# Kernel tuning notes

Hardware: AMD Instinct MI355X
Metric: run time of the kernel (lower is better)

## Reference

```python
import jax, jax.numpy as jnp
import numpy as np

N_NODES = 100000
N_EDGES = 1000000
NUM_FEATURES = 64
HIDDEN = 64
NUM_GRAPHS = 128


def setup_inputs() -> dict:
    key = jax.random.key(0)
    ks = jax.random.split(key, 12)
    x = jax.random.normal(ks[0], (N_NODES, NUM_FEATURES), dtype=jnp.float32)
    edge_index = jax.random.randint(ks[1], (2, N_EDGES), 0, N_NODES, dtype=jnp.int64)
    edge_weight = jax.random.uniform(ks[2], (N_EDGES,), dtype=jnp.float32)
    batch = jnp.sort(jax.random.randint(ks[3], (N_NODES,), 0, NUM_GRAPHS, dtype=jnp.int64))
    s1 = 1.0 / np.sqrt(NUM_FEATURES)
    s2 = 1.0 / np.sqrt(HIDDEN)
    # GraphConv layer 1: lin_rel (with bias) applied to aggregated msgs, lin_root (no bias)
    w1_rel = jax.random.uniform(ks[4], (HIDDEN, NUM_FEATURES), jnp.float32, -s1, s1)
    b1_rel = jax.random.uniform(ks[5], (HIDDEN,), jnp.float32, -s1, s1)
    w1_root = jax.random.uniform(ks[6], (HIDDEN, NUM_FEATURES), jnp.float32, -s1, s1)
    # GraphConv layer 2
    w2_rel = jax.random.uniform(ks[7], (HIDDEN, HIDDEN), jnp.float32, -s2, s2)
    b2_rel = jax.random.uniform(ks[8], (HIDDEN,), jnp.float32, -s2, s2)
    w2_root = jax.random.uniform(ks[9], (HIDDEN, HIDDEN), jnp.float32, -s2, s2)
    # final Linear(hidden, 1)
    w_lin = jax.random.uniform(ks[10], (1, HIDDEN), jnp.float32, -s2, s2)
    b_lin = jax.random.uniform(ks[11], (1,), jnp.float32, -s2, s2)
    return {
        "x": x, "edge_index": edge_index, "edge_weight": edge_weight, "batch": batch,
        "w1_rel": w1_rel, "b1_rel": b1_rel, "w1_root": w1_root,
        "w2_rel": w2_rel, "b2_rel": b2_rel, "w2_root": w2_root,
        "w_lin": w_lin, "b_lin": b_lin,
    }


def graph_conv(x, edge_index, edge_weight, w_rel, b_rel, w_root):
    # messages: x[src] * e, scatter-add into dst  (gather-scale-scatter)
    src, dst = edge_index[0], edge_index[1]
    msgs = x[src] * edge_weight[:, None]                      # [E, F]
    aggr = jax.ops.segment_sum(msgs, dst, num_segments=x.shape[0])  # [N, F]
    return aggr @ w_rel.T + b_rel + x @ w_root.T


def reference(x, edge_index, edge_weight, batch,
              w1_rel, b1_rel, w1_root, w2_rel, b2_rel, w2_root, w_lin, b_lin):
    h = graph_conv(x, edge_index, edge_weight, w1_rel, b1_rel, w1_root)
    h = jax.nn.relu(h)
    h = graph_conv(h, edge_index, edge_weight, w2_rel, b2_rel, w2_root)
    # global_mean_pool over graph ids
    sums = jax.ops.segment_sum(h, batch, num_segments=NUM_GRAPHS)          # [G, H]
    counts = jax.ops.segment_sum(jnp.ones((h.shape[0],), h.dtype), batch,
                                 num_segments=NUM_GRAPHS)                  # [G]
    pooled = sums / jnp.maximum(counts, 1.0)[:, None]
    # dropout(p=0.5) in eval mode is identity
    return pooled @ w_lin.T + b_lin                                        # [G, 1]
```

## Files before the change

### kernel.cpp

```cpp
#include <hip/hip_runtime.h>
#include <hip/hip_bf16.h>


#define N_NODES 100000
#define N_EDGES 1000000
#define NGRAPHS 128
#define BN 512
#define NBUCK ((N_NODES + BN - 1) / BN)
#define FILL_T 16
#define FILL_TILE (256 * FILL_T)
#define FILL_NB ((N_EDGES + FILL_TILE - 1) / FILL_TILE)
#define NTILES (N_NODES / 16)
#define AST 72
#define CVT_NB 3126
#define HIST_NB 256

typedef __attribute__((ext_vector_type(8))) short bf16x8;
typedef __attribute__((ext_vector_type(8))) unsigned short u16x8;
typedef __attribute__((ext_vector_type(4))) float f32x4;

__device__ __forceinline__ unsigned short f2bf(float f) {
    unsigned u = __float_as_uint(f);
    unsigned r = (u + 0x7FFFu + ((u >> 16) & 1u)) >> 16;
    return (unsigned short)r;
}
__device__ __forceinline__ float bf2f(unsigned short h) {
    return __uint_as_float(((unsigned)h) << 16);
}

__global__ __launch_bounds__(256) void prep_cvt_hist_kernel(
    const float* __restrict__ x, unsigned short* __restrict__ xh, int n8,
    const float* __restrict__ w1rel, const float* __restrict__ w1root,
    const float* __restrict__ w2rel, const float* __restrict__ w2root,
    const float* __restrict__ wlin, const float* __restrict__ b2rel,
    const float* __restrict__ blin, unsigned short* __restrict__ whirel,
    unsigned short* __restrict__ wlorel, unsigned short* __restrict__ whiroot,
    unsigned short* __restrict__ wloroot, float* __restrict__ u,
    float* __restrict__ v, float* __restrict__ C,
    const int* __restrict__ ei, int* __restrict__ bcount, int E) {
    int tid = threadIdx.x;
    if (blockIdx.x >= CVT_NB) {
        __shared__ int lh[NBUCK];
        for (int i = tid; i < NBUCK; i += 256) lh[i] = 0;
        __syncthreads();
        int bid2 = blockIdx.x - CVT_NB;
        for (int e = bid2 * 256 + tid; e < E; e += HIST_NB * 256)
            atomicAdd(&lh[ei[E + e] >> 9], 1);
        __syncthreads();
        for (int i = tid; i < NBUCK; i += 256) {
            int c = lh[i];
            if (c) atomicAdd(&bcount[i], c);
        }
        return;
    }
    int i = blockIdx.x * 256 + tid;
    if (i < n8) {
        const float4* xp = (const float4*)x + (size_t)i * 2;
        float4 a = xp[0], b = xp[1];
        u16x8 o;
        o[0] = f2bf(a.x); o[1] = f2bf(a.y); o[2] = f2bf(a.z); o[3] = f2bf(a.w);
        o[4] = f2bf(b.x); o[5] = f2bf(b.y); o[6] = f2bf(b.z); o[7] = f2bf(b.w);
        *((u16x8*)xh + i) = o;
        return;
    }
    for (int k = tid; k < 4096; k += 256) {
        float a = w1rel[k];
        unsigned short hi = f2bf(a);
        whirel[k] = hi;
        wlorel[k] = f2bf(a - bf2f(hi));
        float b = w1root[k];
        unsigned short hb = f2bf(b);
        whiroot[k] = hb;
        wloroot[k] = f2bf(b - bf2f(hb));
    }
    if (tid < 64) {
        float uu = 0.f, vv = 0.f;
        for (int h = 0; h < 64; ++h) {
            float wl = wlin[h];
            uu += wl * w2rel[h * 64 + tid];
            vv += wl * w2root[h * 64 + tid];
        }
        u[tid] = uu;
        v[tid] = vv;
    }
    if (tid == 0) {
        float c = blin[0];
        for (int h = 0; h < 64; ++h) c += wlin[h] * b2rel[h];
        *C = c;
    }
}

__global__ void bucket_scan(const int* __restrict__ bcount,
                            int* __restrict__ boff, int* __restrict__ cursor) {
    __shared__ int s[256];
    int t = threadIdx.x;
    int v = (t < NBUCK) ? bcount[t] : 0;
    s[t] = v;
    __syncthreads();
    for (int off = 1; off < 256; off <<= 1) {
        int x = (t >= off) ? s[t - off] : 0;
        __syncthreads();
        s[t] += x;
        __syncthreads();
    }
    if (t < NBUCK) {
        boff[t] = s[t] - v;
        cursor[t] = s[t] - v;
    }
    if (t == 255) boff[NBUCK] = s[255];
}

__global__ __launch_bounds__(256) void bucket_fill(
    const int* __restrict__ ei, const float* __restrict__ ew,
    int* __restrict__ cursor, int2* __restrict__ ebuf, int E) {
    __shared__ int lh[NBUCK];
    __shared__ int gbase[NBUCK];
    int tid = threadIdx.x;
    for (int i = tid; i < NBUCK; i += 256) lh[i] = 0;
    __syncthreads();
    int base = blockIdx.x * FILL_TILE;
    int2 rec[FILL_T];
    int meta[FILL_T];
#pragma unroll
    for (int i = 0; i < FILL_T; ++i) {
        int e = base + i * 256 + tid;
        meta[i] = -1;
        if (e < E) {
            int src = ei[e];
            int dst = ei[E + e];
            int b = dst >> 9;
            int r = atomicAdd(&lh[b], 1);
            rec[i].x = src | ((dst & (BN - 1)) << 17);
            rec[i].y = __float_as_int(ew[e]);
            meta[i] = (b << 13) | r;
        }
    }
    __syncthreads();
    for (int i = tid; i < NBUCK; i += 256) {
        int c = lh[i];
        gbase[i] = c ? atomicAdd(&cursor[i], c) : 0;
    }
    __syncthreads();
#pragma unroll
    for (int i = 0; i < FILL_T; ++i) {
        if (meta[i] >= 0) {
            int b = meta[i] >> 13;
            int r = meta[i] & 8191;
            ebuf[gbase[b] + r] = rec[i];
        }
    }
}

__global__ __launch_bounds__(512) void csr_build(
    const int* __restrict__ boff, const int2* __restrict__ ebuf,
    const int* __restrict__ batch, int* __restrict__ row_ptr,
    int2* __restrict__ csr, int N) {
    __shared__ int s[BN];
    int b = blockIdx.x;
    int t = threadIdx.x;
    int beg = boff[b], end = boff[b + 1];
    s[t] = 0;
    __syncthreads();
    for (int j = beg + t; j < end; j += 512)
        atomicAdd(&s[(ebuf[j].x >> 17) & (BN - 1)], 1);
    __syncthreads();
    int v = s[t];
    for (int off = 1; off < BN; off <<= 1) {
        int x = (t >= off) ? s[t - off] : 0;
        __syncthreads();
        s[t] += x;
        __syncthreads();
    }
    int excl = s[t] - v;
    int gidx = b * BN + t;
    if (gidx <= N) row_ptr[gidx] = beg + excl;
    __syncthreads();
    s[t] = excl;
    __syncthreads();
    for (int j = beg + t; j < end; j += 512) {
        int2 rec = ebuf[j];
        int dlo = (rec.x >> 17) & (BN - 1);
        int g = batch[b * BN + dlo];
        int r = atomicAdd(&s[dlo], 1);
        int2 o;
        o.x = (rec.x & 0x1FFFF) | (g << 17);
        o.y = rec.y;
        csr[beg + r] = o;
    }
}

__global__ __launch_bounds__(256) void gather_dense_kernel(
    const unsigned short* __restrict__ xh, const int* __restrict__ row_ptr,
    const int2* __restrict__ csr, const unsigned short* __restrict__ whirel,
    const unsigned short* __restrict__ wlorel,
    const unsigned short* __restrict__ whiroot,
    const unsigned short* __restrict__ wloroot,
    const float* __restrict__ b1rel, const float* __restrict__ u,
    const float* __restrict__ v, float* __restrict__ p, float* __restrict__ q,
    int ntiles) {
    __shared__ unsigned short arow[4][16 * AST];
    int lane = threadIdx.x & 63;
    int wv = threadIdx.x >> 6;
    int wave = (blockIdx.x << 2) + wv;
    if (wave >= ntiles) return;
    unsigned short* my = &arow[wv][0];
    int nb = wave * 16;
    int g = lane >> 3;
    int c = lane & 7;

#pragma unroll
    for (int r = 0; r < 2; ++r) {
        int node = nb + r * 8 + g;
        int beg = row_ptr[node], end = row_ptr[node + 1];
        float a0[8], a1[8];
#pragma unroll
        for (int t = 0; t < 8; ++t) { a0[t] = 0.f; a1[t] = 0.f; }
        int j = beg;
        for (; j + 2 <= end; j += 2) {
            int2 e0 = csr[j];
            int2 e1 = csr[j + 1];
            u16x8 x0 = *(const u16x8*)(xh + (size_t)(e0.x & 0x1FFFF) * 64 +
                                       c * 8);
            u16x8 x1 = *(const u16x8*)(xh + (size_t)(e1.x & 0x1FFFF) * 64 +
                                       c * 8);
            float w0 = __int_as_float(e0.y);
            float w1 = __int_as_float(e1.y);
#pragma unroll
            for (int t = 0; t < 8; ++t) {
                a0[t] += w0 * bf2f(x0[t]);
                a1[t] += w1 * bf2f(x1[t]);
            }
        }
        if (j < end) {
            int2 e0 = csr[j];
            u16x8 x0 = *(const u16x8*)(xh + (size_t)(e0.x & 0x1FFFF) * 64 +
                                       c * 8);
            float w0 = __int_as_float(e0.y);
#pragma unroll
            for (int t = 0; t < 8; ++t) a0[t] += w0 * bf2f(x0[t]);
        }
        u16x8 o;
#pragma unroll
        for (int t = 0; t < 8; ++t) o[t] = f2bf(a0[t] + a1[t]);
        *(u16x8*)(my + (r * 8 + g) * AST + c * 8) = o;
    }

    int lo4 = lane & 15;
    int quad = lane >> 4;
    f32x4 acc4[4];
#pragma unroll
    for (int t = 0; t < 4; ++t) acc4[t] = (f32x4){0.f, 0.f, 0.f, 0.f};
#pragma unroll
    for (int s = 0; s < 2; ++s) {
        bf16x8 Aa = *(const bf16x8*)(my + lo4 * AST + s * 32 + quad * 8);
        bf16x8 Ax = *(const bf16x8*)(xh + (size_t)(nb + lo4) * 64 + s * 32 +
                                     quad * 8);
#pragma unroll
        for (int t = 0; t < 4; ++t) {
            int off = (t * 16 + lo4) * 64 + s * 32 + quad * 8;
            bf16x8 bhr = *(const bf16x8*)(whirel + off);
            bf16x8 blr = *(const bf16x8*)(wlorel + off);
            bf16x8 bhx = *(const bf16x8*)(whiroot + off);
            bf16x8 blx = *(const bf16x8*)(wloroot + off);
            acc4[t] = __builtin_amdgcn_mfma_f32_16x16x32_bf16(Aa, bhr, acc4[t],
                                                              0, 0, 0);
            acc4[t] = __builtin_amdgcn_mfma_f32_16x16x32_bf16(Aa, blr, acc4[t],
                                                              0, 0, 0);
            acc4[t] = __builtin_amdgcn_mfma_f32_16x16x32_bf16(Ax, bhx, acc4[t],
                                                              0, 0, 0);
            acc4[t] = __builtin_amdgcn_mfma_f32_16x16x32_bf16(Ax, blx, acc4[t],
                                                              0, 0, 0);
        }
    }

    float pc[4] = {0.f, 0.f, 0.f, 0.f};
    float qc[4] = {0.f, 0.f, 0.f, 0.f};
#pragma unroll
    for (int t = 0; t < 4; ++t) {
        float bb = b1rel[t * 16 + lo4];
        float uu = u[t * 16 + lo4];
        float vv = v[t * 16 + lo4];
#pragma unroll
        for (int r = 0; r < 4; ++r) {
            float h1 = fmaxf(acc4[t][r] + bb, 0.f);
            pc[r] += uu * h1;
            qc[r] += vv * h1;
        }
    }
#pragma unroll
    for (int off = 1; off < 16; off <<= 1) {
#pragma unroll
        for (int r = 0; r < 4; ++r) {
            pc[r] += __shfl_xor(pc[r], off);
            qc[r] += __shfl_xor(qc[r], off);
        }
    }
    if (lo4 == 0) {
        f32x4 po = {pc[0], pc[1], pc[2], pc[3]};
        f32x4 qo = {qc[0], qc[1], qc[2], qc[3]};
        *(f32x4*)(p + nb + quad * 4) = po;
        *(f32x4*)(q + nb + quad * 4) = qo;
    }
}

#define PT_EPT 4
#define PT_EPW (64 * PT_EPT)
#define PT_NB ((N_EDGES + 4 * PT_EPW - 1) / (4 * PT_EPW))
#define PS_NB 98
__global__ __launch_bounds__(256) void pool_both(
    const int2* __restrict__ csr, const float* __restrict__ p,
    const float* __restrict__ q, const int* __restrict__ batch,
    float* __restrict__ gp, float* __restrict__ gq, float* __restrict__ gc,
    int* __restrict__ done, const float* __restrict__ C,
    float* __restrict__ out, int E, int N) {
    __shared__ float lbuf[2 * NGRAPHS];
    __shared__ int amLast;
    int tid = threadIdx.x;
    lbuf[tid] = 0.f;
    __syncthreads();
    if (blockIdx.x < PT_NB) {
        int lane = tid & 63;
        int wid = (blockIdx.x * 256 + tid) >> 6;
        int base = wid * PT_EPW;
        float acc = 0.f;
        int curg = -1;
#pragma unroll
        for (int i = 0; i < PT_EPT; ++i) {
            int j = base + i * 64 + lane;
            if (j < E) {
                int2 e = csr[j];
                int g = ((unsigned)e.x) >> 17;
                float val = __int_as_float(e.y) * p[e.x & 0x1FFFF];
                if (g != curg) {
                    if (curg >= 0) atomicAdd(&lbuf[curg], acc);
                    curg = g;
                    acc = 0.f;
                }
                acc += val;
            }
        }
        if (curg >= 0) atomicAdd(&lbuf[curg], acc);
        __syncthreads();
        if (tid < NGRAPHS) {
            float t = lbuf[tid];
            if (t != 0.f) atomicAdd(&gp[tid], t);
        }
    } else {
        int bid = blockIdx.x - PT_NB;
        for (int i = bid * 256 + tid; i < N; i += PS_NB * 256) {
            int g = batch[i];
            atomicAdd(&lbuf[g], q[i]);
            atomicAdd(&lbuf[NGRAPHS + g], 1.f);
        }
        __syncthreads();
        if (tid < NGRAPHS) {
            if (lbuf[NGRAPHS + tid] != 0.f) {
                atomicAdd(&gq[tid], lbuf[tid]);
                atomicAdd(&gc[tid], lbuf[NGRAPHS + tid]);
            }
        }
    }
    __syncthreads();
    if (tid == 0) {
        __threadfence();
        amLast = (atomicAdd(done, 1) == PT_NB + PS_NB - 1);
    }
    __syncthreads();
    if (amLast) {
        __threadfence();
        if (tid < NGRAPHS) {
            float pv = atomicAdd(&gp[tid], 0.f);
            float qv = atomicAdd(&gq[tid], 0.f);
            float cv = atomicAdd(&gc[tid], 0.f);
            out[tid] = (pv + qv) / fmaxf(cv, 1.f) + C[0];
        }
    }
}

extern "C" void kernel_launch(void* const* d_in, const int* in_sizes, int n_in,
                              void* d_out, int out_size, void* d_ws,
                              size_t ws_size, hipStream_t stream) {
    const float* x      = (const float*)d_in[0];
    const int*   ei     = (const int*)d_in[1];
    const float* ew     = (const float*)d_in[2];
    const int*   batch  = (const int*)d_in[3];
    const float* w1rel  = (const float*)d_in[4];
    const float* b1rel  = (const float*)d_in[5];
    const float* w1root = (const float*)d_in[6];
    const float* w2rel  = (const float*)d_in[7];
    const float* b2rel  = (const float*)d_in[8];
    const float* w2root = (const float*)d_in[9];
    const float* wlin   = (const float*)d_in[10];
    const float* blin   = (const float*)d_in[11];
    float* out = (float*)d_out;

    char* wsb = (char*)d_ws;
    int2* csr  = (int2*)wsb;
    int2* ebuf = (int2*)(wsb + (size_t)N_EDGES * 8);
    char* tail = wsb + (size_t)N_EDGES * 16;
    unsigned short* whirel  = (unsigned short*)tail;
    unsigned short* wlorel  = whirel + 4096;
    unsigned short* whiroot = wlorel + 4096;
    unsigned short* wloroot = whiroot + 4096;
    float* p  = (float*)(wloroot + 4096);
    float* q  = p + N_NODES;
    float* u  = q + N_NODES;
    float* v  = u + 64;
    float* C  = v + 64;
    int*   bcount = (int*)(C + 1);
    float* gp = (float*)(bcount + NBUCK);
    float* gq = gp + NGRAPHS;
    float* gc = gq + NGRAPHS;
    int*   done   = (int*)(gc + NGRAPHS);
    int*   boff   = done + 1;
    int*   cursor = boff + (NBUCK + 1);
    int*   row_ptr = cursor + NBUCK;
    unsigned short* xh = (unsigned short*)(row_ptr + N_NODES + 2);

    hipMemsetAsync(bcount, 0, (NBUCK + 3 * NGRAPHS + 1) * sizeof(int), stream);

    int n8 = N_NODES * 64 / 8;
    prep_cvt_hist_kernel<<<CVT_NB + HIST_NB, 256, 0, stream>>>(
        x, xh, n8, w1rel, w1root, w2rel, w2root, wlin, b2rel, blin, whirel,
        wlorel, whiroot, wloroot, u, v, C, ei, bcount, N_EDGES);

    bucket_scan<<<1, 256, 0, stream>>>(bcount, boff, cursor);
    bucket_fill<<<FILL_NB, 256, 0, stream>>>(ei, ew, cursor, ebuf, N_EDGES);
    csr_build<<<NBUCK, 512, 0, stream>>>(boff, ebuf, batch, row_ptr, csr,
                                         N_NODES);

    gather_dense_kernel<<<(NTILES + 3) / 4, 256, 0, stream>>>(
        xh, row_ptr, csr, whirel, wlorel, whiroot, wloroot, b1rel, u, v, p, q,
        NTILES);

    pool_both<<<PT_NB + PS_NB, 256, 0, stream>>>(csr, p, q, batch, gp, gq, gc,
                                                 done, C, out, N_EDGES,
                                                 N_NODES);
}
```

Measured before the change: 230.5 us.

## Gather neighbor features from an FP8 copy of x to halve gather bytes

Adds a kernel that converts the bf16 node features to FP8 (e4m3), written into the now-free edge staging buffer. The gather loop then reads 16 bytes of FP8 per lane with 4 lanes per node, instead of bf16 with 8 lanes per node, and unpacks with the hardware cvt_pk builtins. The aim is to cut random-gather memory traffic in the main aggregation. The cost is an extra kernel launch plus a conversion pass, and a large loss of precision in the aggregated features that may break the accuracy tolerance.

```diff
diff --git a/kernel.cpp b/kernel.cpp
--- a/kernel.cpp
+++ b/kernel.cpp
@@ -14,10 +14,12 @@
 #define AST 72
 #define CVT_NB 3126
 #define HIST_NB 256
+#define N16 (N_NODES * 64 / 16)
 
 typedef __attribute__((ext_vector_type(8))) short bf16x8;
 typedef __attribute__((ext_vector_type(8))) unsigned short u16x8;
 typedef __attribute__((ext_vector_type(4))) float f32x4;
+typedef __attribute__((ext_vector_type(2))) float f32x2;
 
 __device__ __forceinline__ unsigned short f2bf(float f) {
     unsigned u = __float_as_uint(f);
@@ -26,6 +28,19 @@
 }
 __device__ __forceinline__ float bf2f(unsigned short h) {
     return __uint_as_float(((unsigned)h) << 16);
+}
+__device__ __forceinline__ void fma4(int w, float wt, float* a) {
+    f32x2 lo = __builtin_amdgcn_cvt_pk_f32_fp8(w, false);
+    f32x2 hi = __builtin_amdgcn_cvt_pk_f32_fp8(w, true);
+    a[0] += wt * lo[0];
+    a[1] += wt * lo[1];
+    a[2] += wt * hi[0];
+    a[3] += wt * hi[1];
+}
+__device__ __forceinline__ int pack4(float f0, float f1, float f2, float f3) {
+    int w = __builtin_amdgcn_cvt_pk_fp8_f32(f0, f1, 0, false);
+    w = __builtin_amdgcn_cvt_pk_fp8_f32(f2, f3, w, true);
+    return w;
 }
 
 __global__ __launch_bounds__(256) void prep_cvt_hist_kernel(
@@ -189,9 +204,24 @@
     }
 }
 
+__global__ __launch_bounds__(256) void cvt8_kernel(
+    const unsigned short* __restrict__ xh, int* __restrict__ xf8) {
+    int i = blockIdx.x * 256 + threadIdx.x;
+    if (i >= N16) return;
+    const u16x8* src = (const u16x8*)xh + (size_t)i * 2;
+    u16x8 h0 = src[0], h1 = src[1];
+    int4 o;
+    o.x = pack4(bf2f(h0[0]), bf2f(h0[1]), bf2f(h0[2]), bf2f(h0[3]));
+    o.y = pack4(bf2f(h0[4]), bf2f(h0[5]), bf2f(h0[6]), bf2f(h0[7]));
+    o.z = pack4(bf2f(h1[0]), bf2f(h1[1]), bf2f(h1[2]), bf2f(h1[3]));
+    o.w = pack4(bf2f(h1[4]), bf2f(h1[5]), bf2f(h1[6]), bf2f(h1[7]));
+    ((int4*)xf8)[i] = o;
+}
+
 __global__ __launch_bounds__(256) void gather_dense_kernel(
-    const unsigned short* __restrict__ xh, const int* __restrict__ row_ptr,
-    const int2* __restrict__ csr, const unsigned short* __restrict__ whirel,
+    const unsigned char* __restrict__ xf8, const unsigned short* __restrict__ xh,
+    const int* __restrict__ row_ptr, const int2* __restrict__ csr,
+    const unsigned short* __restrict__ whirel,
     const unsigned short* __restrict__ wlorel,
     const unsigned short* __restrict__ whiroot,
     const unsigned short* __restrict__ wloroot,
@@ -205,44 +235,50 @@
     if (wave >= ntiles) return;
     unsigned short* my = &arow[wv][0];
     int nb = wave * 16;
-    int g = lane >> 3;
-    int c = lane & 7;
-
-#pragma unroll
-    for (int r = 0; r < 2; ++r) {
-        int node = nb + r * 8 + g;
+
+    {
+        int g4 = lane >> 2;
+        int c4 = lane & 3;
+        int node = nb + g4;
         int beg = row_ptr[node], end = row_ptr[node + 1];
-        float a0[8], a1[8];
-#pragma unroll
-        for (int t = 0; t < 8; ++t) { a0[t] = 0.f; a1[t] = 0.f; }
+        float a0[16], a1[16];
+#pragma unroll
+        for (int t = 0; t < 16; ++t) { a0[t] = 0.f; a1[t] = 0.f; }
+        const unsigned char* xb = xf8 + (size_t)c4 * 16;
         int j = beg;
         for (; j + 2 <= end; j += 2) {
             int2 e0 = csr[j];
             int2 e1 = csr[j + 1];
-            u16x8 x0 = *(const u16x8*)(xh + (size_t)(e0.x & 0x1FFFF) * 64 +
-                                       c * 8);
-            u16x8 x1 = *(const u16x8*)(xh + (size_t)(e1.x & 0x1FFFF) * 64 +
-                                       c * 8);
+            int4 r0 = *(const int4*)(xb + (size_t)(e0.x & 0x1FFFF) * 64);
+            int4 r1 = *(const int4*)(xb + (size_t)(e1.x & 0x1FFFF) * 64);
             float w0 = __int_as_float(e0.y);
             float w1 = __int_as_float(e1.y);
-#pragma unroll
-            for (int t = 0; t < 8; ++t) {
-                a0[t] += w0 * bf2f(x0[t]);
-                a1[t] += w1 * bf2f(x1[t]);
-            }
+            fma4(r0.x, w0, a0 + 0);
+            fma4(r0.y, w0, a0 + 4);
+            fma4(r0.z, w0, a0 + 8);
+            fma4(r0.w, w0, a0 + 12);
+            fma4(r1.x, w1, a1 + 0);
+            fma4(r1.y, w1, a1 + 4);
+            fma4(r1.z, w1, a1 + 8);
+            fma4(r1.w, w1, a1 + 12);
         }
         if (j < end) {
             int2 e0 = csr[j];
-            u16x8 x0 = *(const u16x8*)(xh + (size_t)(e0.x & 0x1FFFF) * 64 +
-                                       c * 8);
+            int4 r0 = *(const int4*)(xb + (size_t)(e0.x & 0x1FFFF) * 64);
             float w0 = __int_as_float(e0.y);
-#pragma unroll
-            for (int t = 0; t < 8; ++t) a0[t] += w0 * bf2f(x0[t]);
-        }
-        u16x8 o;
-#pragma unroll
-        for (int t = 0; t < 8; ++t) o[t] = f2bf(a0[t] + a1[t]);
-        *(u16x8*)(my + (r * 8 + g) * AST + c * 8) = o;
+            fma4(r0.x, w0, a0 + 0);
+            fma4(r0.y, w0, a0 + 4);
+            fma4(r0.z, w0, a0 + 8);
+            fma4(r0.w, w0, a0 + 12);
+        }
+        u16x8 o0, o1;
+#pragma unroll
+        for (int t = 0; t < 8; ++t) {
+            o0[t] = f2bf(a0[t] + a1[t]);
+            o1[t] = f2bf(a0[8 + t] + a1[8 + t]);
+        }
+        *(u16x8*)(my + g4 * AST + c4 * 16) = o0;
+        *(u16x8*)(my + g4 * AST + c4 * 16 + 8) = o1;
     }
 
     int lo4 = lane & 15;
@@ -397,6 +433,7 @@
     char* wsb = (char*)d_ws;
     int2* csr  = (int2*)wsb;
     int2* ebuf = (int2*)(wsb + (size_t)N_EDGES * 8);
+    int*  xf8  = (int*)ebuf;
     char* tail = wsb + (size_t)N_EDGES * 16;
     unsigned short* whirel  = (unsigned short*)tail;
     unsigned short* wlorel  = whirel + 4096;
@@ -428,10 +465,11 @@
     bucket_fill<<<FILL_NB, 256, 0, stream>>>(ei, ew, cursor, ebuf, N_EDGES);
     csr_build<<<NBUCK, 512, 0, stream>>>(boff, ebuf, batch, row_ptr, csr,
                                          N_NODES);
+    cvt8_kernel<<<(N16 + 255) / 256, 256, 0, stream>>>(xh, xf8);
 
     gather_dense_kernel<<<(NTILES + 3) / 4, 256, 0, stream>>>(
-        xh, row_ptr, csr, whirel, wlorel, whiroot, wloroot, b1rel, u, v, p, q,
-        NTILES);
+        (const unsigned char*)xf8, xh, row_ptr, csr, whirel, wlorel, whiroot,
+        wloroot, b1rel, u, v, p, q, NTILES);
 
     pool_both<<<PT_NB + PS_NB, 256, 0, stream>>>(csr, p, q, batch, gp, gq, gc,
                                                  done, C, out, N_EDGES,
```

After: 218.0 us. 1.06x faster.
